# Performance work log

Hardware: AMD Instinct MI355X
Metric: run time of the kernel (lower is better)

Reference implementation:

```python
import jax, jax.numpy as jnp
import numpy as np

N = 8192
DISCO_LAMBDA = 0.1
DCORR_POWER = 2  # static, from __init__


def setup_inputs() -> dict:
    key = jax.random.key(0)
    k1, k2, k3, k4 = jax.random.split(key, 4)
    inferences = jax.random.uniform(k1, (N,), dtype=jnp.float32, minval=1e-6, maxval=1.0 - 1e-6)
    labels = jax.random.randint(k2, (N,), 0, 2, dtype=jnp.int32)
    disco_target = jax.random.normal(k3, (N,), dtype=jnp.float32)
    weights = jax.random.uniform(k4, (N,), dtype=jnp.float32)
    return {"inferences": inferences, "labels": labels,
            "disco_target": disco_target, "weights": weights}


def _bce(p, y, w):
    # torch F.binary_cross_entropy: clamps log terms at -100, mean reduction
    logp = jnp.clip(jnp.log(p), -100.0)
    log1mp = jnp.clip(jnp.log1p(-p), -100.0)
    return jnp.mean(w * -(y * logp + (1.0 - y) * log1mp))


def _dcorr(v1, v2, w, mask):
    # mask selects labels==0 subset; zero weights + divide by subset count
    # reproduces torch means over the fancy-indexed subset exactly.
    nf = jnp.sum(mask)                      # subset size (traced scalar)
    wm = w * mask                           # [N]
    amat = jnp.abs(v1[:, None] - v1[None, :])   # [N,N]
    bmat = jnp.abs(v2[:, None] - v2[None, :])   # [N,N]
    a_row = (amat @ wm) / nf                # weighted row means
    b_row = (bmat @ wm) / nf
    a_tot = jnp.dot(a_row, wm) / nf
    b_tot = jnp.dot(b_row, wm) / nf
    Amat = amat - a_row[None, :] - a_row[:, None] + a_tot  # double-centered
    Bmat = bmat - b_row[None, :] - b_row[:, None] + b_tot
    AB = jnp.dot((Amat * Bmat) @ wm, wm) / (nf * nf)
    AA = jnp.dot((Amat * Amat) @ wm, wm) / (nf * nf)
    BB = jnp.dot((Bmat * Bmat) @ wm, wm) / (nf * nf)
    if DCORR_POWER == 1:
        return AB / jnp.sqrt(AA * BB)
    elif DCORR_POWER == 2:
        return AB ** 2 / (AA * BB)
    else:
        return (AB / jnp.sqrt(AA * BB)) ** DCORR_POWER


def reference(inferences, labels, disco_target, weights):
    y = labels.astype(inferences.dtype)
    bce = _bce(inferences, y, weights)
    mask = (labels == 0).astype(inferences.dtype)
    dcorr = _dcorr(inferences, disco_target, weights, mask)
    total = bce + DISCO_LAMBDA * dcorr
    return (total, bce, DISCO_LAMBDA * dcorr)
```

## Files before the change

kernel.cpp:

```cpp
#include <hip/hip_runtime.h>
#include <math.h>

constexpr int N_ELEM = 8192;
constexpr int BLK    = 256;
constexpr int NBLK   = N_ELEM / BLK;
constexpr float LAMBDA = 0.1f;

constexpr int K2_BLK = 256;
constexpr int K2_IPT = 2;
constexpr int K2_IPB = K2_BLK * K2_IPT;
constexpr int K2_GX  = N_ELEM / K2_IPB;
constexpr int K2_JL  = 64;
constexpr int K2_GY  = N_ELEM / K2_JL;


__device__ __forceinline__ float blockReduce(float v, float* sbuf) {
    int tx = threadIdx.x;
    sbuf[tx] = v;
    __syncthreads();
#pragma unroll
    for (int s = BLK / 2; s > 0; s >>= 1) {
        if (tx < s) sbuf[tx] += sbuf[tx + s];
        __syncthreads();
    }
    float r = sbuf[0];
    __syncthreads();
    return r;
}

__global__ void k1_init(const float* __restrict__ inf, const int* __restrict__ lab,
                        const float* __restrict__ tgt, const float* __restrict__ wt,
                        double* __restrict__ dacc, int* __restrict__ cnt,
                        float4* __restrict__ c) {
    __shared__ float sbuf[BLK];
    int i = blockIdx.x * BLK + threadIdx.x;
    float p = inf[i];
    int   y = lab[i];
    float w = wt[i];
    float t = tgt[i];

    float logp   = fmaxf(logf(p),    -100.0f);
    float log1mp = fmaxf(log1pf(-p), -100.0f);
    float yf = (float)y;
    float bce = w * -(yf * logp + (1.0f - yf) * log1mp);

    bool m = (y == 0);
    float wm = m ? w : 0.0f;

    unsigned long long bal = __ballot(m);
    int lane = threadIdx.x & 63;
    int pre  = __popcll(bal & ((1ull << lane) - 1ull));
    int wcnt = __popcll(bal);
    int base = 0;
    if (lane == 0) base = atomicAdd(cnt, wcnt);
    base = __shfl(base, 0);
    if (m) c[base + pre] = make_float4(p, t, w, 0.0f);

    float s;
    s = blockReduce(bce, sbuf);      if (!threadIdx.x) atomicAdd(&dacc[0], (double)s);
    s = blockReduce(wm, sbuf);       if (!threadIdx.x) atomicAdd(&dacc[1], (double)s);
    s = blockReduce(wm * p, sbuf);   if (!threadIdx.x) atomicAdd(&dacc[2], (double)s);
    s = blockReduce(wm * p * p, sbuf); if (!threadIdx.x) atomicAdd(&dacc[3], (double)s);
    s = blockReduce(wm * t, sbuf);   if (!threadIdx.x) atomicAdd(&dacc[4], (double)s);
    s = blockReduce(wm * t * t, sbuf); if (!threadIdx.x) atomicAdd(&dacc[5], (double)s);
}

__global__ void __launch_bounds__(K2_BLK) k2_pairs(
        const float4* __restrict__ c, const int* __restrict__ cnt,
        float* __restrict__ rowA, float* __restrict__ rowB,
        double* __restrict__ dacc) {
    __shared__ float4 sc[K2_JL];
    __shared__ float sbuf[K2_BLK];

    int ncp = (*cnt + (K2_IPB - 1)) & ~(K2_IPB - 1);
    int iBase = blockIdx.x * K2_IPB;
    int jBase = blockIdx.y * K2_JL;
    if (iBase >= ncp || jBase >= ncp) return;

    int tx = threadIdx.x;
    if (tx < K2_JL) sc[tx] = c[jBase + tx];
    int i0 = iBase + tx, i1 = i0 + K2_BLK;
    float4 ci0 = c[i0], ci1 = c[i1];
    __syncthreads();

    float p0 = 0.f, ra0 = 0.f, rb0 = 0.f;
    float p1 = 0.f, ra1 = 0.f, rb1 = 0.f;
#pragma unroll 16
    for (int j = 0; j < K2_JL; ++j) {
        float4 cj = sc[j];
        float d1 = ci0.x - cj.x;
        float d2 = ci0.y - cj.y;
        p0  = fmaf(cj.z, fabsf(d1) * fabsf(d2), p0);
        ra0 = fmaf(cj.z, fabsf(d1), ra0);
        rb0 = fmaf(cj.z, fabsf(d2), rb0);
        float e1 = ci1.x - cj.x;
        float e2 = ci1.y - cj.y;
        p1  = fmaf(cj.z, fabsf(e1) * fabsf(e2), p1);
        ra1 = fmaf(cj.z, fabsf(e1), ra1);
        rb1 = fmaf(cj.z, fabsf(e2), rb1);
    }
    atomicAdd(&rowA[i0], ra0);
    atomicAdd(&rowB[i0], rb0);
    atomicAdd(&rowA[i1], ra1);
    atomicAdd(&rowB[i1], rb1);

    float pb = ci0.z * p0 + ci1.z * p1;
    pb = blockReduce(pb, sbuf);
    if (!tx) atomicAdd(&dacc[6], (double)pb);
}

__global__ void k3_rowmom(const float4* __restrict__ c,
                          const float* __restrict__ rowA, const float* __restrict__ rowB,
                          double* __restrict__ dacc) {
    __shared__ float sbuf[BLK];
    int i = blockIdx.x * BLK + threadIdx.x;
    float w  = c[i].z;
    float ra = rowA[i];
    float rb = rowB[i];
    float s;
    s = blockReduce(w * ra, sbuf);      if (!threadIdx.x) atomicAdd(&dacc[7],  (double)s);
    s = blockReduce(w * ra * ra, sbuf); if (!threadIdx.x) atomicAdd(&dacc[8],  (double)s);
    s = blockReduce(w * rb, sbuf);      if (!threadIdx.x) atomicAdd(&dacc[9],  (double)s);
    s = blockReduce(w * rb * rb, sbuf); if (!threadIdx.x) atomicAdd(&dacc[10], (double)s);
    s = blockReduce(w * ra * rb, sbuf); if (!threadIdx.x) atomicAdd(&dacc[11], (double)s);
}

__global__ void k4_final(const double* __restrict__ dacc, const int* __restrict__ cnt,
                         float* __restrict__ out) {
    double bce = dacc[0] / (double)N_ELEM;
    double nf  = (double)(*cnt);
    double W   = dacc[1];
    double S1a = dacc[2], S2a = dacc[3];
    double S1b = dacc[4], S2b = dacc[5];
    double P   = dacc[6];
    double Ra1 = dacc[7], Ra2 = dacc[8];
    double Rb1 = dacc[9], Rb2 = dacc[10], Rab = dacc[11];

    double n2 = nf * nf, n3 = n2 * nf, n4 = n2 * n2;

    double AAa = 2.0 * (W * S2a - S1a * S1a)
               - 4.0 * Ra2 / nf + 2.0 * W * Ra2 / n2
               + 4.0 * Ra1 * Ra1 / n2 - 4.0 * W * Ra1 * Ra1 / n3
               + W * W * Ra1 * Ra1 / n4;
    double BBa = 2.0 * (W * S2b - S1b * S1b)
               - 4.0 * Rb2 / nf + 2.0 * W * Rb2 / n2
               + 4.0 * Rb1 * Rb1 / n2 - 4.0 * W * Rb1 * Rb1 / n3
               + W * W * Rb1 * Rb1 / n4;
    double ABa = P
               - 4.0 * Rab / nf + 2.0 * W * Rab / n2
               + 4.0 * Ra1 * Rb1 / n2 - 4.0 * W * Ra1 * Rb1 / n3
               + W * W * Ra1 * Rb1 / n4;

    double AB = ABa / n2, AA = AAa / n2, BB = BBa / n2;
    double dcorr = (AB * AB) / (AA * BB);
    double ld = (double)LAMBDA * dcorr;
    out[0] = (float)(bce + ld);
    out[1] = (float)bce;
    out[2] = (float)ld;
}

extern "C" void kernel_launch(void* const* d_in, const int* in_sizes, int n_in,
                              void* d_out, int out_size, void* d_ws, size_t ws_size,
                              hipStream_t stream) {
    const float* inf = (const float*)d_in[0];
    const int*   lab = (const int*)d_in[1];
    const float* tgt = (const float*)d_in[2];
    const float* wt  = (const float*)d_in[3];
    float* out = (float*)d_out;

    double* dacc = (double*)d_ws;
    int*    cnt  = (int*)((char*)d_ws + 128);
    float4* c    = (float4*)((char*)d_ws + 256);
    float*  rowA = (float*)((char*)d_ws + 256 + 16 * N_ELEM);
    float*  rowB = rowA + N_ELEM;

    size_t total = 256 + (size_t)16 * N_ELEM + (size_t)8 * N_ELEM;
    hipMemsetAsync(d_ws, 0, total, stream);

    k1_init<<<NBLK, BLK, 0, stream>>>(inf, lab, tgt, wt, dacc, cnt, c);
    k2_pairs<<<dim3(K2_GX, K2_GY), K2_BLK, 0, stream>>>(c, cnt, rowA, rowB, dacc);
    k3_rowmom<<<NBLK, BLK, 0, stream>>>(c, rowA, rowB, dacc);
    k4_final<<<1, 1, 0, stream>>>(dacc, cnt, out);
}
```

Baseline: 84.78 us.

## Fuse pair pass, row moments and finalize into one kernel with last-block reduction

Restructures the pairwise kernel so each block owns 8 rows and loops over all compacted columns, reducing row sums in-block with wave shuffles instead of atomics into rowA/rowB. Row moments and the final dcorr formula are computed in the same kernel through a last-block-done counter, which removes two launches and most of the memset. Block reductions now use shuffle-based per-block partials written to workspace instead of many double atomics. The trade-offs are 1024 blocks that each re-read the whole column array, and more register pressure from the 8-row unrolled accumulators.

```diff
diff --git a/kernel.cpp b/kernel.cpp
--- a/kernel.cpp
+++ b/kernel.cpp
@@ -6,34 +6,17 @@
 constexpr int NBLK   = N_ELEM / BLK;
 constexpr float LAMBDA = 0.1f;
 
-constexpr int K2_BLK = 256;
-constexpr int K2_IPT = 2;
-constexpr int K2_IPB = K2_BLK * K2_IPT;
-constexpr int K2_GX  = N_ELEM / K2_IPB;
-constexpr int K2_JL  = 64;
-constexpr int K2_GY  = N_ELEM / K2_JL;
-
-
-__device__ __forceinline__ float blockReduce(float v, float* sbuf) {
+constexpr int K2_IPB  = 8;
+constexpr int K2_GRID = N_ELEM / K2_IPB;
+
+
+__global__ void __launch_bounds__(BLK) k1_init(
+        const float* __restrict__ inf, const int* __restrict__ lab,
+        const float* __restrict__ tgt, const float* __restrict__ wt,
+        int* __restrict__ cnt, double* __restrict__ part, float4* __restrict__ c) {
+    __shared__ float red[4][8];
     int tx = threadIdx.x;
-    sbuf[tx] = v;
-    __syncthreads();
-#pragma unroll
-    for (int s = BLK / 2; s > 0; s >>= 1) {
-        if (tx < s) sbuf[tx] += sbuf[tx + s];
-        __syncthreads();
-    }
-    float r = sbuf[0];
-    __syncthreads();
-    return r;
-}
-
-__global__ void k1_init(const float* __restrict__ inf, const int* __restrict__ lab,
-                        const float* __restrict__ tgt, const float* __restrict__ wt,
-                        double* __restrict__ dacc, int* __restrict__ cnt,
-                        float4* __restrict__ c) {
-    __shared__ float sbuf[BLK];
-    int i = blockIdx.x * BLK + threadIdx.x;
+    int i = blockIdx.x * BLK + tx;
     float p = inf[i];
     int   y = lab[i];
     float w = wt[i];
@@ -44,11 +27,11 @@
     float yf = (float)y;
     float bce = w * -(yf * logp + (1.0f - yf) * log1mp);
 
-    bool m = (y == 0);
+    bool  m  = (y == 0);
     float wm = m ? w : 0.0f;
 
     unsigned long long bal = __ballot(m);
-    int lane = threadIdx.x & 63;
+    int lane = tx & 63, wid = tx >> 6;
     int pre  = __popcll(bal & ((1ull << lane) - 1ull));
     int wcnt = __popcll(bal);
     int base = 0;
@@ -56,107 +39,156 @@
     base = __shfl(base, 0);
     if (m) c[base + pre] = make_float4(p, t, w, 0.0f);
 
-    float s;
-    s = blockReduce(bce, sbuf);      if (!threadIdx.x) atomicAdd(&dacc[0], (double)s);
-    s = blockReduce(wm, sbuf);       if (!threadIdx.x) atomicAdd(&dacc[1], (double)s);
-    s = blockReduce(wm * p, sbuf);   if (!threadIdx.x) atomicAdd(&dacc[2], (double)s);
-    s = blockReduce(wm * p * p, sbuf); if (!threadIdx.x) atomicAdd(&dacc[3], (double)s);
-    s = blockReduce(wm * t, sbuf);   if (!threadIdx.x) atomicAdd(&dacc[4], (double)s);
-    s = blockReduce(wm * t * t, sbuf); if (!threadIdx.x) atomicAdd(&dacc[5], (double)s);
+    float v[6] = {bce, wm, wm * p, wm * p * p, wm * t, wm * t * t};
+#pragma unroll
+    for (int k = 0; k < 6; ++k) {
+        float s = v[k];
+#pragma unroll
+        for (int d = 32; d > 0; d >>= 1) s += __shfl_xor(s, d);
+        if (lane == 0) red[wid][k] = s;
+    }
+    __syncthreads();
+    if (tx < 6) {
+        double s = (double)red[0][tx] + (double)red[1][tx]
+                 + (double)red[2][tx] + (double)red[3][tx];
+        part[blockIdx.x * 8 + tx] = s;
+    }
 }
 
-__global__ void __launch_bounds__(K2_BLK) k2_pairs(
+__global__ void __launch_bounds__(BLK) k2_pairs(
         const float4* __restrict__ c, const int* __restrict__ cnt,
-        float* __restrict__ rowA, float* __restrict__ rowB,
-        double* __restrict__ dacc) {
-    __shared__ float4 sc[K2_JL];
-    __shared__ float sbuf[K2_BLK];
-
-    int ncp = (*cnt + (K2_IPB - 1)) & ~(K2_IPB - 1);
+        int* __restrict__ done, double* __restrict__ gpart,
+        const double* __restrict__ part, float* __restrict__ out) {
+    __shared__ float4 si[K2_IPB];
+    __shared__ float red[4][24];
+    __shared__ float totS[24];
+    __shared__ int lastFlag;
+
+    int tx = threadIdx.x;
+    int lane = tx & 63, wid = tx >> 6;
+    int nc = *cnt;
     int iBase = blockIdx.x * K2_IPB;
-    int jBase = blockIdx.y * K2_JL;
-    if (iBase >= ncp || jBase >= ncp) return;
-
-    int tx = threadIdx.x;
-    if (tx < K2_JL) sc[tx] = c[jBase + tx];
-    int i0 = iBase + tx, i1 = i0 + K2_BLK;
-    float4 ci0 = c[i0], ci1 = c[i1];
+    double* myg = gpart + (size_t)blockIdx.x * 8;
+
+    if (iBase < nc) {
+        if (tx < K2_IPB) si[tx] = c[iBase + tx];
+        __syncthreads();
+        float xi[K2_IPB], yi[K2_IPB];
+#pragma unroll
+        for (int k = 0; k < K2_IPB; ++k) { xi[k] = si[k].x; yi[k] = si[k].y; }
+
+        float ra[K2_IPB] = {0}, rb[K2_IPB] = {0}, pp[K2_IPB] = {0};
+        int iters = (nc + BLK - 1) >> 8;
+#pragma unroll 2
+        for (int j0 = 0; j0 < iters; ++j0) {
+            int j = j0 * BLK + tx;
+            float4 cj = c[j];
+            float uj = (j < nc) ? cj.z : 0.0f;
+#pragma unroll
+            for (int k = 0; k < K2_IPB; ++k) {
+                float f1 = fabsf(xi[k] - cj.x);
+                float f2 = fabsf(yi[k] - cj.y);
+                ra[k] = fmaf(uj, f1, ra[k]);
+                rb[k] = fmaf(uj, f2, rb[k]);
+                pp[k] = fmaf(uj, f1 * f2, pp[k]);
+            }
+        }
+#pragma unroll
+        for (int k = 0; k < K2_IPB; ++k) {
+            float s0 = ra[k], s1 = rb[k], s2 = pp[k];
+#pragma unroll
+            for (int d = 32; d > 0; d >>= 1) {
+                s0 += __shfl_xor(s0, d);
+                s1 += __shfl_xor(s1, d);
+                s2 += __shfl_xor(s2, d);
+            }
+            if (lane == 0) { red[wid][k] = s0; red[wid][8 + k] = s1; red[wid][16 + k] = s2; }
+        }
+        __syncthreads();
+        if (tx < 24)
+            totS[tx] = red[0][tx] + red[1][tx] + red[2][tx] + red[3][tx];
+        __syncthreads();
+        if (tx == 0) {
+            double P = 0, Ra1 = 0, Ra2 = 0, Rb1 = 0, Rb2 = 0, Rab = 0;
+#pragma unroll
+            for (int k = 0; k < K2_IPB; ++k) {
+                double w   = (iBase + k < nc) ? (double)si[k].z : 0.0;
+                double rak = totS[k], rbk = totS[8 + k], ppk = totS[16 + k];
+                Ra1 += w * rak;        Ra2 += w * rak * rak;
+                Rb1 += w * rbk;        Rb2 += w * rbk * rbk;
+                Rab += w * rak * rbk;  P   += w * ppk;
+            }
+            myg[0] = P; myg[1] = Ra1; myg[2] = Ra2;
+            myg[3] = Rb1; myg[4] = Rb2; myg[5] = Rab;
+        }
+    } else {
+        if (tx == 0) {
+            myg[0] = 0; myg[1] = 0; myg[2] = 0; myg[3] = 0; myg[4] = 0; myg[5] = 0;
+        }
+    }
+
+    __threadfence();
+    if (tx == 0) {
+        int old = atomicAdd(done, 1);
+        lastFlag = (old == K2_GRID - 1);
+    }
     __syncthreads();
-
-    float p0 = 0.f, ra0 = 0.f, rb0 = 0.f;
-    float p1 = 0.f, ra1 = 0.f, rb1 = 0.f;
-#pragma unroll 16
-    for (int j = 0; j < K2_JL; ++j) {
-        float4 cj = sc[j];
-        float d1 = ci0.x - cj.x;
-        float d2 = ci0.y - cj.y;
-        p0  = fmaf(cj.z, fabsf(d1) * fabsf(d2), p0);
-        ra0 = fmaf(cj.z, fabsf(d1), ra0);
-        rb0 = fmaf(cj.z, fabsf(d2), rb0);
-        float e1 = ci1.x - cj.x;
-        float e2 = ci1.y - cj.y;
-        p1  = fmaf(cj.z, fabsf(e1) * fabsf(e2), p1);
-        ra1 = fmaf(cj.z, fabsf(e1), ra1);
-        rb1 = fmaf(cj.z, fabsf(e2), rb1);
-    }
-    atomicAdd(&rowA[i0], ra0);
-    atomicAdd(&rowB[i0], rb0);
-    atomicAdd(&rowA[i1], ra1);
-    atomicAdd(&rowB[i1], rb1);
-
-    float pb = ci0.z * p0 + ci1.z * p1;
-    pb = blockReduce(pb, sbuf);
-    if (!tx) atomicAdd(&dacc[6], (double)pb);
-}
-
-__global__ void k3_rowmom(const float4* __restrict__ c,
-                          const float* __restrict__ rowA, const float* __restrict__ rowB,
-                          double* __restrict__ dacc) {
-    __shared__ float sbuf[BLK];
-    int i = blockIdx.x * BLK + threadIdx.x;
-    float w  = c[i].z;
-    float ra = rowA[i];
-    float rb = rowB[i];
-    float s;
-    s = blockReduce(w * ra, sbuf);      if (!threadIdx.x) atomicAdd(&dacc[7],  (double)s);
-    s = blockReduce(w * ra * ra, sbuf); if (!threadIdx.x) atomicAdd(&dacc[8],  (double)s);
-    s = blockReduce(w * rb, sbuf);      if (!threadIdx.x) atomicAdd(&dacc[9],  (double)s);
-    s = blockReduce(w * rb * rb, sbuf); if (!threadIdx.x) atomicAdd(&dacc[10], (double)s);
-    s = blockReduce(w * ra * rb, sbuf); if (!threadIdx.x) atomicAdd(&dacc[11], (double)s);
-}
-
-__global__ void k4_final(const double* __restrict__ dacc, const int* __restrict__ cnt,
-                         float* __restrict__ out) {
-    double bce = dacc[0] / (double)N_ELEM;
-    double nf  = (double)(*cnt);
-    double W   = dacc[1];
-    double S1a = dacc[2], S2a = dacc[3];
-    double S1b = dacc[4], S2b = dacc[5];
-    double P   = dacc[6];
-    double Ra1 = dacc[7], Ra2 = dacc[8];
-    double Rb1 = dacc[9], Rb2 = dacc[10], Rab = dacc[11];
-
-    double n2 = nf * nf, n3 = n2 * nf, n4 = n2 * n2;
-
-    double AAa = 2.0 * (W * S2a - S1a * S1a)
-               - 4.0 * Ra2 / nf + 2.0 * W * Ra2 / n2
-               + 4.0 * Ra1 * Ra1 / n2 - 4.0 * W * Ra1 * Ra1 / n3
-               + W * W * Ra1 * Ra1 / n4;
-    double BBa = 2.0 * (W * S2b - S1b * S1b)
-               - 4.0 * Rb2 / nf + 2.0 * W * Rb2 / n2
-               + 4.0 * Rb1 * Rb1 / n2 - 4.0 * W * Rb1 * Rb1 / n3
-               + W * W * Rb1 * Rb1 / n4;
-    double ABa = P
-               - 4.0 * Rab / nf + 2.0 * W * Rab / n2
-               + 4.0 * Ra1 * Rb1 / n2 - 4.0 * W * Ra1 * Rb1 / n3
-               + W * W * Ra1 * Rb1 / n4;
-
-    double AB = ABa / n2, AA = AAa / n2, BB = BBa / n2;
-    double dcorr = (AB * AB) / (AA * BB);
-    double ld = (double)LAMBDA * dcorr;
-    out[0] = (float)(bce + ld);
-    out[1] = (float)bce;
-    out[2] = (float)ld;
+    if (!lastFlag) return;
+
+    __shared__ double dred[4][6];
+    double acc[6] = {0, 0, 0, 0, 0, 0};
+    for (int r = tx; r < K2_GRID; r += BLK) {
+        const double* gp = gpart + (size_t)r * 8;
+#pragma unroll
+        for (int k = 0; k < 6; ++k) acc[k] += gp[k];
+    }
+#pragma unroll
+    for (int k = 0; k < 6; ++k) {
+        double s = acc[k];
+#pragma unroll
+        for (int d = 32; d > 0; d >>= 1) s += __shfl_xor(s, d);
+        if (lane == 0) dred[wid][k] = s;
+    }
+    __syncthreads();
+    if (tx == 0) {
+        double P   = dred[0][0] + dred[1][0] + dred[2][0] + dred[3][0];
+        double Ra1 = dred[0][1] + dred[1][1] + dred[2][1] + dred[3][1];
+        double Ra2 = dred[0][2] + dred[1][2] + dred[2][2] + dred[3][2];
+        double Rb1 = dred[0][3] + dred[1][3] + dred[2][3] + dred[3][3];
+        double Rb2 = dred[0][4] + dred[1][4] + dred[2][4] + dred[3][4];
+        double Rab = dred[0][5] + dred[1][5] + dred[2][5] + dred[3][5];
+
+        double bceS = 0, W = 0, S1a = 0, S2a = 0, S1b = 0, S2b = 0;
+        for (int b = 0; b < NBLK; ++b) {
+            const double* pb = part + b * 8;
+            bceS += pb[0]; W += pb[1]; S1a += pb[2];
+            S2a += pb[3]; S1b += pb[4]; S2b += pb[5];
+        }
+
+        double nf = (double)nc;
+        double n2 = nf * nf, n3 = n2 * nf, n4 = n2 * n2;
+
+        double AAa = 2.0 * (W * S2a - S1a * S1a)
+                   - 4.0 * Ra2 / nf + 2.0 * W * Ra2 / n2
+                   + 4.0 * Ra1 * Ra1 / n2 - 4.0 * W * Ra1 * Ra1 / n3
+                   + W * W * Ra1 * Ra1 / n4;
+        double BBa = 2.0 * (W * S2b - S1b * S1b)
+                   - 4.0 * Rb2 / nf + 2.0 * W * Rb2 / n2
+                   + 4.0 * Rb1 * Rb1 / n2 - 4.0 * W * Rb1 * Rb1 / n3
+                   + W * W * Rb1 * Rb1 / n4;
+        double ABa = P
+                   - 4.0 * Rab / nf + 2.0 * W * Rab / n2
+                   + 4.0 * Ra1 * Rb1 / n2 - 4.0 * W * Ra1 * Rb1 / n3
+                   + W * W * Ra1 * Rb1 / n4;
+
+        double AB = ABa / n2, AA = AAa / n2, BB = BBa / n2;
+        double dcorr = (AB * AB) / (AA * BB);
+        double ld = (double)LAMBDA * dcorr;
+        double bce = bceS / (double)N_ELEM;
+        out[0] = (float)(bce + ld);
+        out[1] = (float)bce;
+        out[2] = (float)ld;
+    }
 }
 
 extern "C" void kernel_launch(void* const* d_in, const int* in_sizes, int n_in,
@@ -168,17 +200,13 @@
     const float* wt  = (const float*)d_in[3];
     float* out = (float*)d_out;
 
-    double* dacc = (double*)d_ws;
-    int*    cnt  = (int*)((char*)d_ws + 128);
-    float4* c    = (float4*)((char*)d_ws + 256);
-    float*  rowA = (float*)((char*)d_ws + 256 + 16 * N_ELEM);
-    float*  rowB = rowA + N_ELEM;
-
-    size_t total = 256 + (size_t)16 * N_ELEM + (size_t)8 * N_ELEM;
-    hipMemsetAsync(d_ws, 0, total, stream);
-
-    k1_init<<<NBLK, BLK, 0, stream>>>(inf, lab, tgt, wt, dacc, cnt, c);
-    k2_pairs<<<dim3(K2_GX, K2_GY), K2_BLK, 0, stream>>>(c, cnt, rowA, rowB, dacc);
-    k3_rowmom<<<NBLK, BLK, 0, stream>>>(c, rowA, rowB, dacc);
-    k4_final<<<1, 1, 0, stream>>>(dacc, cnt, out);
+    int*    cnt   = (int*)d_ws;
+    int*    done  = cnt + 1;
+    double* part  = (double*)((char*)d_ws + 256);
+    double* gpart = (double*)((char*)d_ws + 4096);
+    float4* c     = (float4*)((char*)d_ws + 4096 + (size_t)K2_GRID * 8 * sizeof(double));
+
+    hipMemsetAsync(d_ws, 0, 256, stream);
+    k1_init<<<NBLK, BLK, 0, stream>>>(inf, lab, tgt, wt, cnt, part, c);
+    k2_pairs<<<K2_GRID, BLK, 0, stream>>>(c, cnt, done, gpart, part, out);
 }
```

Measured after the change: 140.0 us. 1.65x slower.
